# Performance work log

Measured on AMD Instinct MI355X. Metric: run time of the kernel, lower is better.

Reference implementation:

```python
import jax, jax.numpy as jnp
import numpy as np

B, G, I, E = 256, 24, 512, 512


def setup_inputs() -> dict:
    key = jax.random.key(0)
    k1, k2 = jax.random.split(key)
    inp = jax.random.normal(k1, (B, G, I), dtype=jnp.float32)
    weights = jax.random.normal(k2, (G, I, E), dtype=jnp.float32) * (1.0 / np.sqrt(E))
    bias = 0.1 * jnp.ones((E,), dtype=jnp.float32)
    # Cyclic group inverse-index table: row h is the permutation g -> (g - h) mod G,
    # matching symmetry_group.index2inverse_indices[h] (each row a valid permutation).
    g_ar = np.arange(G)
    inv_indices = jnp.asarray((g_ar[None, :] - g_ar[:, None]) % G, dtype=jnp.int32)
    return {"input": inp, "weights": weights, "bias": bias, "inv_indices": inv_indices}


def reference(input, weights, bias, inv_indices):
    # conv_filter[h, g, i, e] = weights[inv_indices[h, g], i, e]   -> [G, G, I, E]
    conv_filter = weights[inv_indices]
    # (input[:,None,:,:,None] * filter[None]).sum(2).sum(2) == einsum over g, i
    out = jnp.einsum("bgi,hgie->bhe", input, conv_filter)  # [B, G, E]
    return out + bias
```

## Files before the change

kernel.cpp:

```cpp
#include <hip/hip_runtime.h>
#include <hip/hip_bf16.h>
#include <stdint.h>

#define G_ 24
#define B_ 256
#define I_ 512
#define E_ 512
#define K_ (G_ * I_)
#define SPLITK 5

typedef __hip_bfloat16 bf16;
typedef __bf16 bf16x8 __attribute__((ext_vector_type(8)));
typedef float f32x4 __attribute__((ext_vector_type(4)));

__global__ void cvt_in_kernel(const float* __restrict__ in, bf16* __restrict__ out, int n4) {
  int idx = blockIdx.x * blockDim.x + threadIdx.x;
  if (idx >= n4) return;
  float4 v = reinterpret_cast<const float4*>(in)[idx];
  union { bf16 h[4]; uint2 u; } pk;
  pk.h[0] = __float2bfloat16(v.x);
  pk.h[1] = __float2bfloat16(v.y);
  pk.h[2] = __float2bfloat16(v.z);
  pk.h[3] = __float2bfloat16(v.w);
  reinterpret_cast<uint2*>(out)[idx] = pk.u;
}

__global__ void transpose_w_kernel(const float* __restrict__ W, bf16* __restrict__ Wt) {
  __shared__ float tile[32][33];
  const int g = blockIdx.z;
  const int i0 = blockIdx.x * 32;
  const int e0 = blockIdx.y * 32;
  const float* src = W + (size_t)g * (I_ * E_) + (size_t)(i0 + threadIdx.y) * E_ + e0 + threadIdx.x;
  #pragma unroll
  for (int r = 0; r < 32; r += 8)
    tile[threadIdx.y + r][threadIdx.x] = src[(size_t)r * E_];
  __syncthreads();
  bf16* dst = Wt + (size_t)g * (I_ * E_) + (size_t)(e0 + threadIdx.y) * I_ + i0 + threadIdx.x;
  #pragma unroll
  for (int r = 0; r < 32; r += 8)
    dst[(size_t)r * I_] = __float2bfloat16(tile[threadIdx.x][threadIdx.y + r]);
}

__global__ void init_out_kernel(const float* __restrict__ bias, float* __restrict__ out, int n4) {
  int idx = blockIdx.x * blockDim.x + threadIdx.x;
  if (idx >= n4) return;
  int e4 = idx & 127;
  reinterpret_cast<float4*>(out)[idx] = reinterpret_cast<const float4*>(bias)[e4];
}


#define FENCE() asm volatile("" ::: "memory")
#define BAR()   __builtin_amdgcn_s_barrier()
#define LGKM0() do { asm volatile("s_waitcnt lgkmcnt(0)" ::: "memory"); \
                     __builtin_amdgcn_sched_barrier(0); } while (0)
#define VMW(N)  asm volatile("s_waitcnt vmcnt(" #N ")" ::: "memory")

__device__ __forceinline__ void gload16(const bf16* g, bf16* l) {
  __builtin_amdgcn_global_load_lds((const __attribute__((address_space(1))) void*)g,
                                   (__attribute__((address_space(3))) void*)l, 16, 0, 0);
}

__global__ __launch_bounds__(512, 2) void gemm256_kernel(
    const bf16* __restrict__ A,
    const bf16* __restrict__ Wt,
    float* __restrict__ out) {

  __shared__ __align__(16) bf16 lds[2][2][256 * 64];

  const int tid  = threadIdx.x;
  const int lane = tid & 63;
  const int wave = tid >> 6;
  const int wr   = wave >> 2;
  const int wc   = wave & 3;
  const int rsel = lane & 15;
  const int q    = lane >> 4;

  const int h     = blockIdx.z / SPLITK;
  const int split = blockIdx.z % SPLITK;
  const int n0    = blockIdx.x * 256;

  const int T0 = split * 38 + (split < 2 ? split : 2);
  const int NT = 38 + (split < 2 ? 1 : 0);

  f32x4 acc[8][4];
  #pragma unroll
  for (int i = 0; i < 8; ++i)
    #pragma unroll
    for (int j = 0; j < 4; ++j)
      acc[i][j] = (f32x4){0.f, 0.f, 0.f, 0.f};

  auto stageA = [&](int t, int half, int b) {
    const bf16* Ab = A + (size_t)t * 64;
    #pragma unroll
    for (int j = 0; j < 2; ++j) {
      int quarter = half + j * 2;
      int row  = quarter * 64 + (tid >> 3);
      int slot = (tid & 7) ^ ((tid >> 3) & 7);
      gload16(Ab + (size_t)row * K_ + slot * 8,
              &lds[b][0][(size_t)(quarter * 512 + tid) * 8]);
    }
  };
  auto stageB = [&](int t, int half, int b) {
    int g = t >> 3, i0 = (t & 7) * 64;
    int gsrc = g - h; if (gsrc < 0) gsrc += G_;
    const bf16* Wb = Wt + (size_t)gsrc * (I_ * E_) + (size_t)n0 * I_ + i0;
    #pragma unroll
    for (int j = 0; j < 2; ++j) {
      int u    = j * 512 + tid;
      int band = u >> 8;
      int rowb = band * 64 + half * 32 + ((u >> 3) & 31);
      int slot = (u & 7) ^ ((u >> 3) & 7);
      gload16(Wb + (size_t)rowb * I_ + slot * 8,
              &lds[b][1][(size_t)(rowb * 8 + (u & 7)) * 8]);
    }
  };

  bf16x8 af[8];
  bf16x8 b0f[4];
  bf16x8 b1f[4];
  auto readA = [&](int mhalf, int b, bf16x8* dst) {
    const bf16* p = &lds[b][0][0];
    #pragma unroll
    for (int mi = 0; mi < 4; ++mi) {
      int r   = wr * 128 + (mhalf * 4 + mi) * 16 + rsel;
      int off = r * 64 + (q ^ (r & 7)) * 8;
      dst[mi * 2 + 0] = *(const bf16x8*)(p + off);
      dst[mi * 2 + 1] = *(const bf16x8*)(p + (off ^ 32));
    }
  };
  auto readB = [&](int nhalf, int b, bf16x8* dst) {
    const bf16* p = &lds[b][1][0];
    #pragma unroll
    for (int ni = 0; ni < 2; ++ni) {
      int r   = wc * 64 + (nhalf * 2 + ni) * 16 + rsel;
      int off = r * 64 + (q ^ (r & 7)) * 8;
      dst[ni * 2 + 0] = *(const bf16x8*)(p + off);
      dst[ni * 2 + 1] = *(const bf16x8*)(p + (off ^ 32));
    }
  };
  auto MMA = [&](int miB, int niB, bf16x8* a, bf16x8* bb) {
    #pragma unroll
    for (int kk = 0; kk < 2; ++kk)
      #pragma unroll
      for (int mi = 0; mi < 4; ++mi)
        #pragma unroll
        for (int ni = 0; ni < 2; ++ni)
          acc[miB + mi][niB + ni] = __builtin_amdgcn_mfma_f32_16x16x32_bf16(
              a[mi * 2 + kk], bb[ni * 2 + kk], acc[miB + mi][niB + ni], 0, 0, 0);
  };

#define KTILE(T, S1A, S1B, S2A, S2B, VMPH0, VMPH3) do {                         \
                                           \
    if (S1A) stageA((T) + 1, 1, buf ^ 1);                                       \
    readA(0, buf, af); readB(0, buf, b0f);                                      \
    FENCE(); BAR(); LGKM0();                                                    \
    __builtin_amdgcn_s_setprio(1); MMA(0, 0, af, b0f); __builtin_amdgcn_s_setprio(0); \
    VMPH0; FENCE(); BAR();                                                      \
                                                    \
    if (S1B) stageB((T) + 1, 1, buf ^ 1);                                       \
    readB(1, buf, b1f);                                                         \
    FENCE(); BAR(); LGKM0();                                                    \
    __builtin_amdgcn_s_setprio(1); MMA(0, 2, af, b1f); __builtin_amdgcn_s_setprio(0); \
    FENCE(); BAR();                                                             \
                                                    \
    if (S2A) stageA((T) + 2, 0, buf);                                           \
    readA(1, buf, af);                                                          \
    FENCE(); BAR(); LGKM0();                                                    \
    __builtin_amdgcn_s_setprio(1); MMA(4, 2, af, b1f); __builtin_amdgcn_s_setprio(0); \
    FENCE(); BAR();                                                             \
                                                    \
    if (S2B) stageB((T) + 2, 0, buf);                                           \
    FENCE(); BAR();                                                             \
    __builtin_amdgcn_s_setprio(1); MMA(4, 0, af, b0f); __builtin_amdgcn_s_setprio(0); \
    VMPH3; FENCE(); BAR();                                                      \
    buf ^= 1;                                                                   \
  } while (0)

  stageA(T0, 0, 0); stageB(T0, 0, 0);
  stageA(T0, 1, 0); stageB(T0, 1, 0);
  stageA(T0 + 1, 0, 1); stageB(T0 + 1, 0, 1);
  VMW(8);
  FENCE(); BAR();

  int buf = 0;
  for (int lt = 0; lt + 2 < NT; ++lt) {
    KTILE(T0 + lt, true, true, true, true, VMW(6), VMW(8));
  }
  KTILE(T0 + NT - 2, true, true, false, false, VMW(6), VMW(4));
  KTILE(T0 + NT - 1, false, false, false, false, VMW(0), ((void)0));

#undef KTILE

  #pragma unroll
  for (int mi = 0; mi < 8; ++mi) {
    #pragma unroll
    for (int ni = 0; ni < 4; ++ni) {
      int ecol  = n0 + wc * 64 + ni * 16 + (lane & 15);
      int brow0 = wr * 128 + mi * 16 + (lane >> 4) * 4;
      float* o = out + (size_t)brow0 * (G_ * E_) + (size_t)h * E_ + ecol;
      #pragma unroll
      for (int r = 0; r < 4; ++r)
        atomicAdd(o + (size_t)r * (G_ * E_), acc[mi][ni][r]);
    }
  }
}

extern "C" void kernel_launch(void* const* d_in, const int* in_sizes, int n_in,
                              void* d_out, int out_size, void* d_ws, size_t ws_size,
                              hipStream_t stream) {
  const float* in   = (const float*)d_in[0];
  const float* w    = (const float*)d_in[1];
  const float* bias = (const float*)d_in[2];
  float* out = (float*)d_out;

  bf16* A_bf = (bf16*)d_ws;
  bf16* Wt   = (bf16*)((char*)d_ws + (size_t)B_ * K_ * 2);

  const int n4in  = (B_ * K_) / 4;
  const int n4out = (B_ * G_ * E_) / 4;
  cvt_in_kernel<<<n4in / 256, 256, 0, stream>>>(in, A_bf, n4in);
  transpose_w_kernel<<<dim3(E_ / 32, I_ / 32, G_), dim3(32, 8), 0, stream>>>(w, Wt);
  init_out_kernel<<<n4out / 256, 256, 0, stream>>>(bias, out, n4out);
  gemm256_kernel<<<dim3(E_ / 256, 1, G_ * SPLITK), 512, 0, stream>>>(A_bf, Wt, out);
}
```

Baseline: 132.5 us.

## Use split-K of 4 with interleaved k-tile order and flattened grid

Changes split-K from 5 to 4 so each block handles 48 k-tiles, and flattens the grid into 192 one-dimensional blocks where neighbouring blocks share h and split. The k-tile order is permuted so that blocks processing the same 64-column K slice at the same time touch overlapping A and weight rows, aiming for better L2/MALL reuse across concurrently running blocks. It also removes the uneven split remainder handling. The risk is fewer blocks than the previous 240, which lowers parallelism on a machine with 256 CUs, in exchange for fewer atomic output passes.

```diff
diff --git a/kernel.cpp b/kernel.cpp
--- a/kernel.cpp
+++ b/kernel.cpp
@@ -7,7 +7,8 @@
 #define I_ 512
 #define E_ 512
 #define K_ (G_ * I_)
-#define SPLITK 5
+#define SPLITK 4
+#define NT 48
 
 typedef __hip_bfloat16 bf16;
 typedef __bf16 bf16x8 __attribute__((ext_vector_type(8)));
@@ -48,7 +49,6 @@
   reinterpret_cast<float4*>(out)[idx] = reinterpret_cast<const float4*>(bias)[e4];
 }
 
-
 #define FENCE() asm volatile("" ::: "memory")
 #define BAR()   __builtin_amdgcn_s_barrier()
 #define LGKM0() do { asm volatile("s_waitcnt lgkmcnt(0)" ::: "memory"); \
@@ -75,12 +75,13 @@
   const int rsel = lane & 15;
   const int q    = lane >> 4;
 
-  const int h     = blockIdx.z / SPLITK;
-  const int split = blockIdx.z % SPLITK;
-  const int n0    = blockIdx.x * 256;
-
-  const int T0 = split * 38 + (split < 2 ? split : 2);
-  const int NT = 38 + (split < 2 ? 1 : 0);
+  const int bid = blockIdx.x;
+  const int x   = bid & 7;
+  const int h   = bid >> 3;
+  const int n0  = (x & 1) * 256;
+  const int s   = x >> 1;
+
+  auto tt = [&](int lt) { return (s * 6 + lt % 6) * 8 + lt / 6; };
 
   f32x4 acc[8][4];
   #pragma unroll
@@ -149,46 +150,52 @@
               a[mi * 2 + kk], bb[ni * 2 + kk], acc[miB + mi][niB + ni], 0, 0, 0);
   };
 
-#define KTILE(T, S1A, S1B, S2A, S2B, VMPH0, VMPH3) do {                         \
+#define KTILE(T1, T2, S1A, S1B, S2A, S2B, VMPH0, VMPH3) do {                    \
                                            \
-    if (S1A) stageA((T) + 1, 1, buf ^ 1);                                       \
+    if (S1A) stageA((T1), 1, buf ^ 1);                                          \
     readA(0, buf, af); readB(0, buf, b0f);                                      \
     FENCE(); BAR(); LGKM0();                                                    \
     __builtin_amdgcn_s_setprio(1); MMA(0, 0, af, b0f); __builtin_amdgcn_s_setprio(0); \
     VMPH0; FENCE(); BAR();                                                      \
                                                     \
-    if (S1B) stageB((T) + 1, 1, buf ^ 1);                                       \
+    if (S1B) stageB((T1), 1, buf ^ 1);                                          \
     readB(1, buf, b1f);                                                         \
     FENCE(); BAR(); LGKM0();                                                    \
     __builtin_amdgcn_s_setprio(1); MMA(0, 2, af, b1f); __builtin_amdgcn_s_setprio(0); \
     FENCE(); BAR();                                                             \
                                                     \
-    if (S2A) stageA((T) + 2, 0, buf);                                           \
+    if (S2A) stageA((T2), 0, buf);                                              \
     readA(1, buf, af);                                                          \
     FENCE(); BAR(); LGKM0();                                                    \
     __builtin_amdgcn_s_setprio(1); MMA(4, 2, af, b1f); __builtin_amdgcn_s_setprio(0); \
     FENCE(); BAR();                                                             \
                                                     \
-    if (S2B) stageB((T) + 2, 0, buf);                                           \
+    if (S2B) stageB((T2), 0, buf);                                              \
     FENCE(); BAR();                                                             \
     __builtin_amdgcn_s_setprio(1); MMA(4, 0, af, b0f); __builtin_amdgcn_s_setprio(0); \
     VMPH3; FENCE(); BAR();                                                      \
     buf ^= 1;                                                                   \
   } while (0)
 
-  stageA(T0, 0, 0); stageB(T0, 0, 0);
-  stageA(T0, 1, 0); stageB(T0, 1, 0);
-  stageA(T0 + 1, 0, 1); stageB(T0 + 1, 0, 1);
-  VMW(8);
-  FENCE(); BAR();
+  {
+    const int t0 = tt(0), t1 = tt(1);
+    stageA(t0, 0, 0); stageB(t0, 0, 0);
+    stageA(t0, 1, 0); stageB(t0, 1, 0);
+    stageA(t1, 0, 1); stageB(t1, 0, 1);
+    VMW(8);
+    FENCE(); BAR();
+  }
 
   int buf = 0;
   for (int lt = 0; lt + 2 < NT; ++lt) {
-    KTILE(T0 + lt, true, true, true, true, VMW(6), VMW(8));
-  }
-  KTILE(T0 + NT - 2, true, true, false, false, VMW(6), VMW(4));
-  KTILE(T0 + NT - 1, false, false, false, false, VMW(0), ((void)0));
-
+    const int t1 = tt(lt + 1), t2 = tt(lt + 2);
+    KTILE(t1, t2, true, true, true, true, VMW(6), VMW(8));
+  }
+  {
+    const int tl = tt(NT - 1);
+    KTILE(tl, 0, true, true, false, false, VMW(6), VMW(4));
+    KTILE(0, 0, false, false, false, false, VMW(0), ((void)0));
+  }
 #undef KTILE
 
   #pragma unroll
@@ -221,5 +228,5 @@
   cvt_in_kernel<<<n4in / 256, 256, 0, stream>>>(in, A_bf, n4in);
   transpose_w_kernel<<<dim3(E_ / 32, I_ / 32, G_), dim3(32, 8), 0, stream>>>(w, Wt);
   init_out_kernel<<<n4out / 256, 256, 0, stream>>>(bias, out, n4out);
-  gemm256_kernel<<<dim3(E_ / 256, 1, G_ * SPLITK), 512, 0, stream>>>(A_bf, Wt, out);
-}
+  gemm256_kernel<<<192, 512, 0, stream>>>(A_bf, Wt, out);
+}
```

After: 139.4 us. 5.3% more time.
